# Kernel tuning notes

Measured on AMD Instinct MI355X. Metric: run time of the kernel, lower is better.

The kernel has to match this reference:

```python
import jax, jax.numpy as jnp
import numpy as np

B, S, D, H = 4, 2048, 1024, 16
DK = D // H


def setup_inputs() -> dict:
    key = jax.random.key(0)
    ks = jax.random.split(key, 12)
    s = 1.0 / np.sqrt(D)
    return {
        "query": jax.random.normal(ks[0], (B, S, D), jnp.float32),
        "key": jax.random.normal(ks[1], (B, S, D), jnp.float32),
        "value": jax.random.normal(ks[2], (B, S, D), jnp.float32),
        "mask": jnp.ones((1, 1, S, S), jnp.int32),
        "w_q": jax.random.normal(ks[3], (D, D), jnp.float32) * s,
        "b_q": jax.random.normal(ks[4], (D,), jnp.float32) * s,
        "w_k": jax.random.normal(ks[5], (D, D), jnp.float32) * s,
        "b_k": jax.random.normal(ks[6], (D,), jnp.float32) * s,
        "w_v": jax.random.normal(ks[7], (D, D), jnp.float32) * s,
        "b_v": jax.random.normal(ks[8], (D,), jnp.float32) * s,
        "w_o": jax.random.normal(ks[9], (D, D), jnp.float32) * s,
        "b_o": jax.random.normal(ks[10], (D,), jnp.float32) * s,
    }


def reference(query, key, value, mask, w_q, b_q, w_k, b_k, w_v, b_v, w_o, b_o):
    # linear projections (torch Linear: x @ W^T + b)
    q = query @ w_q.T + b_q
    k = key @ w_k.T + b_k
    v = value @ w_v.T + b_v
    # [B, S, D] -> [B, H, S, DK]
    q = q.reshape(B, S, H, DK).transpose(0, 2, 1, 3)
    k = k.reshape(B, S, H, DK).transpose(0, 2, 1, 3)
    v = v.reshape(B, S, H, DK).transpose(0, 2, 1, 3)
    scores = jnp.einsum("bhqd,bhkd->bhqk", q, k) / jnp.sqrt(jnp.float32(DK))
    scores = jnp.where(mask == 0, jnp.float32(-1e9), scores)
    attn = jax.nn.softmax(scores, axis=-1)  # dropout p=0.0 -> identity
    x = jnp.einsum("bhqk,bhkd->bhqd", attn, v)
    x = x.transpose(0, 2, 1, 3).reshape(B, S, D)
    return x @ w_o.T + b_o
```

## Files before the change

kernel.cpp:

```cpp
#include <hip/hip_runtime.h>
#include <stdint.h>

#define S_LEN 2048
#define NHEAD 16
#define DHEAD 64
#define DMODEL 1024
#define MROWS 8192

typedef unsigned short ushort_t;
typedef __attribute__((ext_vector_type(8))) __bf16 bf16x8;
typedef __attribute__((ext_vector_type(4))) float f32x4;

__device__ __forceinline__ float bf2f(ushort_t h) {
    union { unsigned int u; float f; } v; v.u = ((unsigned int)h) << 16; return v.f;
}
__device__ __forceinline__ ushort_t f2bf(float f) {
    union { float f; unsigned int u; } v; v.f = f;
    unsigned int u = v.u + 0x7fffu + ((v.u >> 16) & 1u);
    return (ushort_t)(u >> 16);
}

__device__ __forceinline__ void gload_lds16(const void* g, void* l)
{
    auto* g1 = reinterpret_cast<const __attribute__((address_space(1))) void*>(
        reinterpret_cast<uintptr_t>(g));
    auto* l3 = reinterpret_cast<__attribute__((address_space(3))) void*>(
        reinterpret_cast<uintptr_t>(l));
    __builtin_amdgcn_global_load_lds(g1, l3, 16, 0, 0);
}

__global__ void detect_dtype(const unsigned int* __restrict__ q, int* __restrict__ flag)
{
    __shared__ int cnt;
    if (threadIdx.x == 0) cnt = 0;
    __syncthreads();
    int c = 0;
    for (int i = 0; i < 8; ++i) {
        const unsigned int w = q[threadIdx.x * 8 + i];
        const unsigned int lo = w & 0xffffu;
        const unsigned int e = (lo >> 7) & 0xffu;
        if (lo == 0u || (e >= 96u && e <= 160u)) ++c;
    }
    atomicAdd(&cnt, c);
    __syncthreads();
    if (threadIdx.x == 0) flag[0] = (cnt < 400) ? 1 : 0;
}

__global__ void mask_flags(const int* __restrict__ mask, int* __restrict__ flags)
{
    __shared__ int ok_s;
    if (threadIdx.x == 0) ok_s = 1;
    __syncthreads();
    const int t = blockIdx.x;
    const int tq = t >> 4, tk = t & 15;
    int ok = 1;
    for (int i = 0; i < 64; ++i) {
        const int idx = i * 256 + threadIdx.x;
        const int r = idx >> 7, c = idx & 127;
        if (mask[(size_t)(tq * 128 + r) * S_LEN + tk * 128 + c] == 0) { ok = 0; break; }
    }
    if (!ok) atomicAnd(&ok_s, 0);
    __syncthreads();
    if (threadIdx.x == 0) flags[t] = ok_s;
}

__device__ __forceinline__ float loadscal(const void* b, int i, bool f32)
{
    return f32 ? ((const float*)b)[i] : bf2f(((const ushort_t*)b)[i]);
}

__global__ __launch_bounds__(256)
void conv_bf16(const void* __restrict__ src, ushort_t* __restrict__ dst,
               int n8, const int* __restrict__ dflag, int fidx)
{
    const bool f32 = dflag[fidx] != 0;
    const int stride = gridDim.x * 256;
    for (int i = blockIdx.x * 256 + threadIdx.x; i < n8; i += stride) {
        if (f32) {
            const float4 a = ((const float4*)src)[2 * (size_t)i];
            const float4 b = ((const float4*)src)[2 * (size_t)i + 1];
            union { ushort_t u[8]; uint4 v; } p;
            p.u[0] = f2bf(a.x); p.u[1] = f2bf(a.y); p.u[2] = f2bf(a.z); p.u[3] = f2bf(a.w);
            p.u[4] = f2bf(b.x); p.u[5] = f2bf(b.y); p.u[6] = f2bf(b.z); p.u[7] = f2bf(b.w);
            ((uint4*)dst)[i] = p.v;
        } else {
            ((uint4*)dst)[i] = ((const uint4*)src)[i];
        }
    }
}

template <bool OUTF>
__global__ __launch_bounds__(256, 2)
void gemm_bf16(const ushort_t* __restrict__ A, const ushort_t* __restrict__ W,
               const void* __restrict__ bias, void* __restrict__ out,
               const int* __restrict__ dflag)
{
    constexpr int K = DMODEL, N = DMODEL;
    __shared__ ushort_t As[128 * 32];
    __shared__ ushort_t Bs[128 * 32];
    const bool bf32 = dflag[1] != 0;
    const int tid = threadIdx.x;
    const int lane = tid & 63;
    const int wave = tid >> 6;
    const int lrow = lane & 15, lq = lane >> 4;
    const int m0 = blockIdx.x * 128;
    const int n0 = blockIdx.y * 128;
    const int wr = (wave >> 1) * 64;
    const int wc = (wave & 1) * 64;

    const f32x4 zero4 = {0.f, 0.f, 0.f, 0.f};
    f32x4 acc[4][4];
#pragma unroll
    for (int i = 0; i < 4; ++i)
#pragma unroll
        for (int j = 0; j < 4; ++j) acc[i][j] = zero4;

    for (int k0 = 0; k0 < K; k0 += 32) {
#pragma unroll
        for (int i = 0; i < 2; ++i) {
            const int c = tid + i * 256;
            const int r = c >> 2, cc = (c & 3) * 8;
            const int lb = (wave * 64 + i * 256) * 8;
            gload_lds16(&A[(size_t)(m0 + r) * K + k0 + cc], &As[lb]);
            gload_lds16(&W[(size_t)(n0 + r) * K + k0 + cc], &Bs[lb]);
        }
        __syncthreads();
        bf16x8 af[4], bfr[4];
#pragma unroll
        for (int t = 0; t < 4; ++t) {
            af[t]  = *(const bf16x8*)(&As[(wr + t * 16 + lrow) * 32 + lq * 8]);
            bfr[t] = *(const bf16x8*)(&Bs[(wc + t * 16 + lrow) * 32 + lq * 8]);
        }
#pragma unroll
        for (int mt = 0; mt < 4; ++mt)
#pragma unroll
            for (int nt = 0; nt < 4; ++nt)
                acc[mt][nt] = __builtin_amdgcn_mfma_f32_16x16x32_bf16(
                    af[mt], bfr[nt], acc[mt][nt], 0, 0, 0);
        __syncthreads();
    }

#pragma unroll
    for (int nt = 0; nt < 4; ++nt) {
        const int n = n0 + wc + nt * 16 + lrow;
        const float bv = loadscal(bias, n, bf32);
#pragma unroll
        for (int mt = 0; mt < 4; ++mt) {
            const int mbase = m0 + wr + mt * 16 + lq * 4;
#pragma unroll
            for (int r = 0; r < 4; ++r) {
                const float v = acc[mt][nt][r] + bv;
                const size_t o = (size_t)(mbase + r) * N + n;
                if (OUTF) ((float*)out)[o] = v;
                else      ((ushort_t*)out)[o] = f2bf(v);
            }
        }
    }
}

__global__ __launch_bounds__(256, 2)
void attn_mfma(const ushort_t* __restrict__ Q, const ushort_t* __restrict__ K,
               const ushort_t* __restrict__ V, const int* __restrict__ mask,
               const int* __restrict__ flags, ushort_t* __restrict__ X)
{
    constexpr int KP = 72;
    constexpr int VP = 130;
    constexpr int PP = 72;
    __shared__ ushort_t Ks[128 * KP];
    __shared__ ushort_t VTs[64 * VP];
    __shared__ ushort_t Ps[4][32 * PP];

    const int tid = threadIdx.x;
    const int lane = tid & 63;
    const int wave = tid >> 6;
    const int lrow = lane & 15, lq = lane >> 4;
    const int bh = blockIdx.y, b = bh >> 4, h = bh & 15;
    const int q0 = blockIdx.x * 128;
    const int qw = q0 + wave * 32;
    const int coff = h * 64;
    const size_t rowb = (size_t)b * S_LEN;

    bf16x8 qf[2][2];
#pragma unroll
    for (int mt = 0; mt < 2; ++mt)
#pragma unroll
        for (int ks = 0; ks < 2; ++ks)
            qf[mt][ks] = *(const bf16x8*)(
                &Q[(rowb + qw + mt * 16 + lrow) * DMODEL + coff + ks * 32 + lq * 8]);

    const f32x4 zero4 = {0.f, 0.f, 0.f, 0.f};
    f32x4 o[2][4];
    float mr[2][4], lr[2][4];
#pragma unroll
    for (int mt = 0; mt < 2; ++mt) {
#pragma unroll
        for (int nt = 0; nt < 4; ++nt) o[mt][nt] = zero4;
#pragma unroll
        for (int r = 0; r < 4; ++r) { mr[mt][r] = -1e30f; lr[mt][r] = 0.f; }
    }

    ushort_t* const pw = &Ps[wave][0];

    for (int kt = 0; kt < 16; ++kt) {
        const int k0 = kt * 128;
#pragma unroll
        for (int i = 0; i < 4; ++i) {
            const int c = tid + i * 256;
            const int r = c >> 3, cc = (c & 7) * 8;
            *(uint4*)(&Ks[r * KP + cc]) =
                *(const uint4*)(&K[(rowb + k0 + r) * DMODEL + coff + cc]);
        }
#pragma unroll
        for (int i = 0; i < 2; ++i) {
            const int c = tid + i * 256;
            const int k2 = c >> 3;
            const int cc = (c & 7) * 8;
            union { uint4 v; ushort_t u[8]; } a, bb;
            a.v  = *(const uint4*)(&V[(rowb + k0 + 2 * k2)     * DMODEL + coff + cc]);
            bb.v = *(const uint4*)(&V[(rowb + k0 + 2 * k2 + 1) * DMODEL + coff + cc]);
#pragma unroll
            for (int j = 0; j < 8; ++j) {
                const unsigned int pk = (unsigned int)a.u[j] | ((unsigned int)bb.u[j] << 16);
                *(unsigned int*)(&VTs[(cc + j) * VP + 2 * k2]) = pk;
            }
        }
        __syncthreads();

        f32x4 s[2][8];
#pragma unroll
        for (int mt = 0; mt < 2; ++mt)
#pragma unroll
            for (int nt = 0; nt < 8; ++nt) s[mt][nt] = zero4;
#pragma unroll
        for (int nt = 0; nt < 8; ++nt) {
#pragma unroll
            for (int ks = 0; ks < 2; ++ks) {
                const bf16x8 kf = *(const bf16x8*)(&Ks[(nt * 16 + lrow) * KP + ks * 32 + lq * 8]);
                s[0][nt] = __builtin_amdgcn_mfma_f32_16x16x32_bf16(qf[0][ks], kf, s[0][nt], 0, 0, 0);
                s[1][nt] = __builtin_amdgcn_mfma_f32_16x16x32_bf16(qf[1][ks], kf, s[1][nt], 0, 0, 0);
            }
        }

#pragma unroll
        for (int mt = 0; mt < 2; ++mt)
#pragma unroll
            for (int nt = 0; nt < 8; ++nt)
#pragma unroll
                for (int r = 0; r < 4; ++r) s[mt][nt][r] *= 0.125f;
        if (!flags[blockIdx.x * 16 + kt]) {
            for (int mt = 0; mt < 2; ++mt)
                for (int nt = 0; nt < 8; ++nt)
                    for (int r = 0; r < 4; ++r) {
                        const int qi = qw + mt * 16 + lq * 4 + r;
                        const int ki = k0 + nt * 16 + lrow;
                        if (mask[(size_t)qi * S_LEN + ki] == 0) s[mt][nt][r] = -1e9f;
                    }
        }

#pragma unroll
        for (int mt = 0; mt < 2; ++mt) {
#pragma unroll
            for (int r = 0; r < 4; ++r) {
                float v = s[mt][0][r];
#pragma unroll
                for (int nt = 1; nt < 8; ++nt) v = fmaxf(v, s[mt][nt][r]);
#pragma unroll
                for (int off = 1; off < 16; off <<= 1) v = fmaxf(v, __shfl_xor(v, off, 64));
                const float mn = fmaxf(mr[mt][r], v);
                const float alpha = __expf(mr[mt][r] - mn);
                mr[mt][r] = mn;
                float rs = 0.f;
#pragma unroll
                for (int nt = 0; nt < 8; ++nt) {
                    const float p = __expf(s[mt][nt][r] - mn);
                    s[mt][nt][r] = p;
                    rs += p;
                }
#pragma unroll
                for (int off = 1; off < 16; off <<= 1) rs += __shfl_xor(rs, off, 64);
                lr[mt][r] = lr[mt][r] * alpha + rs;
#pragma unroll
                for (int nt = 0; nt < 4; ++nt) o[mt][nt][r] *= alpha;
            }
        }

#pragma unroll
        for (int half = 0; half < 2; ++half) {
#pragma unroll
            for (int mt = 0; mt < 2; ++mt)
#pragma unroll
                for (int nt = 0; nt < 4; ++nt)
#pragma unroll
                    for (int r = 0; r < 4; ++r)
                        pw[(mt * 16 + lq * 4 + r) * PP + nt * 16 + lrow] =
                            f2bf(s[mt][half * 4 + nt][r]);
#pragma unroll
            for (int ks = 0; ks < 2; ++ks) {
                const bf16x8 pf0 = *(const bf16x8*)(&pw[lrow * PP + ks * 32 + lq * 8]);
                const bf16x8 pf1 = *(const bf16x8*)(&pw[(16 + lrow) * PP + ks * 32 + lq * 8]);
                const int kb = half * 64 + ks * 32;
#pragma unroll
                for (int nt = 0; nt < 4; ++nt) {
                    const bf16x8 vf = *(const bf16x8*)(
                        &VTs[(nt * 16 + lrow) * VP + kb + lq * 8]);
                    o[0][nt] = __builtin_amdgcn_mfma_f32_16x16x32_bf16(pf0, vf, o[0][nt], 0, 0, 0);
                    o[1][nt] = __builtin_amdgcn_mfma_f32_16x16x32_bf16(pf1, vf, o[1][nt], 0, 0, 0);
                }
            }
        }
        __syncthreads();
    }

#pragma unroll
    for (int mt = 0; mt < 2; ++mt) {
#pragma unroll
        for (int r = 0; r < 4; ++r) {
            const float inv = 1.f / lr[mt][r];
            const int si = qw + mt * 16 + lq * 4 + r;
#pragma unroll
            for (int nt = 0; nt < 4; ++nt) {
                const int dk = nt * 16 + lrow;
                X[(rowb + si) * DMODEL + coff + dk] = f2bf(o[mt][nt][r] * inv);
            }
        }
    }
}

extern "C" void kernel_launch(void* const* d_in, const int* in_sizes, int n_in,
                              void* d_out, int out_size, void* d_ws, size_t ws_size,
                              hipStream_t stream)
{
    const void* query = d_in[0];
    const void* key   = d_in[1];
    const void* value = d_in[2];
    const int*  mask  = (const int*)d_in[3];
    const void* w_q = d_in[4];
    const void* b_q = d_in[5];
    const void* w_k = d_in[6];
    const void* b_k = d_in[7];
    const void* w_v = d_in[8];
    const void* b_v = d_in[9];
    const void* w_o = d_in[10];
    const void* b_o = d_in[11];

    const size_t TEN = (size_t)MROWS * DMODEL;
    ushort_t* Kp = (ushort_t*)d_ws;
    ushort_t* Vp = Kp + TEN;
    ushort_t* Xp = Vp + TEN;
    int* dflag   = (int*)(Xp + TEN);
    int* flags   = dflag + 2;
    ushort_t* Qp = (ushort_t*)d_out;
    ushort_t* Ac = Qp + TEN;
    ushort_t* Wq_c = Vp;
    ushort_t* Wk_c = Vp + (size_t)DMODEL * DMODEL;
    ushort_t* Wv_c = Xp;
    ushort_t* Wo_c = Vp;

    const int WN8 = DMODEL * DMODEL / 8;
    const int AN8 = (int)(TEN / 8);

    detect_dtype<<<1, 64, 0, stream>>>((const unsigned int*)query, dflag + 0);
    detect_dtype<<<1, 64, 0, stream>>>((const unsigned int*)w_q,   dflag + 1);
    mask_flags<<<256, 256, 0, stream>>>(mask, flags);

    conv_bf16<<<512, 256, 0, stream>>>(w_q, Wq_c, WN8, dflag, 1);
    conv_bf16<<<512, 256, 0, stream>>>(w_k, Wk_c, WN8, dflag, 1);
    conv_bf16<<<512, 256, 0, stream>>>(w_v, Wv_c, WN8, dflag, 1);

    const dim3 gg(64, 8);
    conv_bf16<<<2048, 256, 0, stream>>>(query, Ac, AN8, dflag, 0);
    gemm_bf16<false><<<gg, 256, 0, stream>>>(Ac, Wq_c, b_q, Qp, dflag);
    conv_bf16<<<2048, 256, 0, stream>>>(key, Ac, AN8, dflag, 0);
    gemm_bf16<false><<<gg, 256, 0, stream>>>(Ac, Wk_c, b_k, Kp, dflag);
    conv_bf16<<<2048, 256, 0, stream>>>(value, Ac, AN8, dflag, 0);
    gemm_bf16<false><<<gg, 256, 0, stream>>>(Ac, Wv_c, b_v, Vp, dflag);

    attn_mfma<<<dim3(16, 64), 256, 0, stream>>>(Qp, Kp, Vp, mask, flags, Xp);

    conv_bf16<<<512, 256, 0, stream>>>(w_o, Wo_c, WN8, dflag, 1);
    gemm_bf16<true><<<gg, 256, 0, stream>>>(Xp, Wo_c, b_o, d_out, dflag);
}
```

Measured before the change: 515.6 us.

## Double-buffer GEMM LDS tiles, fold softmax scale into exp2, raise attention occupancy

The projection GEMM gets two LDS buffers per operand, so the next K tile is loaded while the current one feeds the MFMAs, and each K tile now needs one barrier instead of two. Both kernels wrap their MFMA bursts in s_setprio to favour matrix issue. In attention, the separate 0.125 multiply is removed: the 1/sqrt(dk) scale and log2(e) are folded into one constant used with hardware exp2. The P-tile row padding goes from 72 to 68. The attention launch bound rises from 2 to 3 blocks per CU. Risks: the new 136-byte P-row stride leaves the 16-byte LDS fragment reads only 8-byte aligned, and the higher occupancy target may force register spills.

Measured after the change: 581.2 us. 1.13x slower.

```diff
diff --git a/kernel.cpp b/kernel.cpp
--- a/kernel.cpp
+++ b/kernel.cpp
@@ -96,8 +96,8 @@
                const int* __restrict__ dflag)
 {
     constexpr int K = DMODEL, N = DMODEL;
-    __shared__ ushort_t As[128 * 32];
-    __shared__ ushort_t Bs[128 * 32];
+    __shared__ ushort_t As[2][128 * 32];
+    __shared__ ushort_t Bs[2][128 * 32];
     const bool bf32 = dflag[1] != 0;
     const int tid = threadIdx.x;
     const int lane = tid & 63;
@@ -115,28 +115,44 @@
 #pragma unroll
         for (int j = 0; j < 4; ++j) acc[i][j] = zero4;
 
-    for (int k0 = 0; k0 < K; k0 += 32) {
-#pragma unroll
-        for (int i = 0; i < 2; ++i) {
-            const int c = tid + i * 256;
-            const int r = c >> 2, cc = (c & 3) * 8;
-            const int lb = (wave * 64 + i * 256) * 8;
-            gload_lds16(&A[(size_t)(m0 + r) * K + k0 + cc], &As[lb]);
-            gload_lds16(&W[(size_t)(n0 + r) * K + k0 + cc], &Bs[lb]);
-        }
-        __syncthreads();
+    const int r0  = tid >> 2;
+    const int cc0 = (tid & 3) * 8;
+    const int lb  = wave * 64 * 8;
+    const int lb1 = (wave * 64 + 256) * 8;
+
+    auto stage = [&](int buf, int k0) __attribute__((always_inline)) {
+        gload_lds16(&A[(size_t)(m0 + r0) * K + k0 + cc0],      &As[buf][lb]);
+        gload_lds16(&W[(size_t)(n0 + r0) * K + k0 + cc0],      &Bs[buf][lb]);
+        gload_lds16(&A[(size_t)(m0 + r0 + 64) * K + k0 + cc0], &As[buf][lb1]);
+        gload_lds16(&W[(size_t)(n0 + r0 + 64) * K + k0 + cc0], &Bs[buf][lb1]);
+    };
+    auto compute = [&](int buf) __attribute__((always_inline)) {
         bf16x8 af[4], bfr[4];
 #pragma unroll
         for (int t = 0; t < 4; ++t) {
-            af[t]  = *(const bf16x8*)(&As[(wr + t * 16 + lrow) * 32 + lq * 8]);
-            bfr[t] = *(const bf16x8*)(&Bs[(wc + t * 16 + lrow) * 32 + lq * 8]);
-        }
+            af[t]  = *(const bf16x8*)(&As[buf][(wr + t * 16 + lrow) * 32 + lq * 8]);
+            bfr[t] = *(const bf16x8*)(&Bs[buf][(wc + t * 16 + lrow) * 32 + lq * 8]);
+        }
+        __builtin_amdgcn_s_setprio(1);
 #pragma unroll
         for (int mt = 0; mt < 4; ++mt)
 #pragma unroll
             for (int nt = 0; nt < 4; ++nt)
                 acc[mt][nt] = __builtin_amdgcn_mfma_f32_16x16x32_bf16(
                     af[mt], bfr[nt], acc[mt][nt], 0, 0, 0);
+        __builtin_amdgcn_s_setprio(0);
+    };
+
+    stage(0, 0);
+    __syncthreads();
+#pragma unroll 1
+    for (int tt = 0; tt < 16; ++tt) {
+        const int t0 = 2 * tt;
+        stage(1, (t0 + 1) * 32);
+        compute(0);
+        __syncthreads();
+        if (tt < 15) stage(0, (t0 + 2) * 32);
+        compute(1);
         __syncthreads();
     }
 
@@ -158,14 +174,15 @@
     }
 }
 
-__global__ __launch_bounds__(256, 2)
+__global__ __launch_bounds__(256, 3)
 void attn_mfma(const ushort_t* __restrict__ Q, const ushort_t* __restrict__ K,
                const ushort_t* __restrict__ V, const int* __restrict__ mask,
                const int* __restrict__ flags, ushort_t* __restrict__ X)
 {
     constexpr int KP = 72;
     constexpr int VP = 130;
-    constexpr int PP = 72;
+    constexpr int PP = 68;
+    constexpr float CEXP = 0.18033688f;
     __shared__ ushort_t Ks[128 * KP];
     __shared__ ushort_t VTs[64 * VP];
     __shared__ ushort_t Ps[4][32 * PP];
@@ -231,6 +248,7 @@
         for (int mt = 0; mt < 2; ++mt)
 #pragma unroll
             for (int nt = 0; nt < 8; ++nt) s[mt][nt] = zero4;
+        __builtin_amdgcn_s_setprio(1);
 #pragma unroll
         for (int nt = 0; nt < 8; ++nt) {
 #pragma unroll
@@ -240,13 +258,8 @@
                 s[1][nt] = __builtin_amdgcn_mfma_f32_16x16x32_bf16(qf[1][ks], kf, s[1][nt], 0, 0, 0);
             }
         }
-
-#pragma unroll
-        for (int mt = 0; mt < 2; ++mt)
-#pragma unroll
-            for (int nt = 0; nt < 8; ++nt)
-#pragma unroll
-                for (int r = 0; r < 4; ++r) s[mt][nt][r] *= 0.125f;
+        __builtin_amdgcn_s_setprio(0);
+
         if (!flags[blockIdx.x * 16 + kt]) {
             for (int mt = 0; mt < 2; ++mt)
                 for (int nt = 0; nt < 8; ++nt)
@@ -261,18 +274,19 @@
         for (int mt = 0; mt < 2; ++mt) {
 #pragma unroll
             for (int r = 0; r < 4; ++r) {
-                float v = s[mt][0][r];
-#pragma unroll
-                for (int nt = 1; nt < 8; ++nt) v = fmaxf(v, s[mt][nt][r]);
+                float v = fmaxf(
+                    fmaxf(fmaxf(s[mt][0][r], s[mt][1][r]), fmaxf(s[mt][2][r], s[mt][3][r])),
+                    fmaxf(fmaxf(s[mt][4][r], s[mt][5][r]), fmaxf(s[mt][6][r], s[mt][7][r])));
 #pragma unroll
                 for (int off = 1; off < 16; off <<= 1) v = fmaxf(v, __shfl_xor(v, off, 64));
                 const float mn = fmaxf(mr[mt][r], v);
-                const float alpha = __expf(mr[mt][r] - mn);
+                const float alpha = __builtin_amdgcn_exp2f((mr[mt][r] - mn) * CEXP);
                 mr[mt][r] = mn;
+                const float mnC = mn * CEXP;
                 float rs = 0.f;
 #pragma unroll
                 for (int nt = 0; nt < 8; ++nt) {
-                    const float p = __expf(s[mt][nt][r] - mn);
+                    const float p = __builtin_amdgcn_exp2f(fmaf(s[mt][nt][r], CEXP, -mnC));
                     s[mt][nt][r] = p;
                     rs += p;
                 }
@@ -299,6 +313,7 @@
                 const bf16x8 pf0 = *(const bf16x8*)(&pw[lrow * PP + ks * 32 + lq * 8]);
                 const bf16x8 pf1 = *(const bf16x8*)(&pw[(16 + lrow) * PP + ks * 32 + lq * 8]);
                 const int kb = half * 64 + ks * 32;
+                __builtin_amdgcn_s_setprio(1);
 #pragma unroll
                 for (int nt = 0; nt < 4; ++nt) {
                     const bf16x8 vf = *(const bf16x8*)(
@@ -306,6 +321,7 @@
                     o[0][nt] = __builtin_amdgcn_mfma_f32_16x16x32_bf16(pf0, vf, o[0][nt], 0, 0, 0);
                     o[1][nt] = __builtin_amdgcn_mfma_f32_16x16x32_bf16(pf1, vf, o[1][nt], 0, 0, 0);
                 }
+                __builtin_amdgcn_s_setprio(0);
             }
         }
         __syncthreads();
```
